# Kernel optimization log

Hardware: AMD Instinct MI355X
Metric: run time of the kernel (lower is better)

## Reference

```python
import jax, jax.numpy as jnp
import numpy as np

N = 100000      # nodes
E = 1600000     # edges (avg degree 16)
F_IN = 128      # dataset.num_features
H = 64          # hidden_channels
C = 40          # dataset.num_classes
LAYERS = 4      # number_conv_layers
EPS = 1e-12     # F.normalize eps


def _agnn_layer(x, src, dst):
    # AGNNConv with beta=1 (requires_grad=False):
    # alpha_ij = softmax_i( cos(x_i, x_j) ), out_i = sum_j alpha_ij * x_j
    xn = x / jnp.maximum(jnp.linalg.norm(x, axis=1, keepdims=True), EPS)
    logits = jnp.sum(xn[dst] * xn[src], axis=1)                      # [E]
    m = jax.lax.stop_gradient(jax.ops.segment_max(logits, dst, num_segments=N))
    e = jnp.exp(logits - m[dst])
    s = jax.ops.segment_sum(e, dst, num_segments=N)
    alpha = e / s[dst]                                               # [E]
    return jax.ops.segment_sum(alpha[:, None] * x[src], dst, num_segments=N)


def setup_inputs() -> dict:
    key = jax.random.key(0)
    k = jax.random.split(key, 6)
    x = jax.random.normal(k[0], (N, F_IN), dtype=jnp.float32)
    edge_index = jax.random.randint(k[1], (2, E), 0, N, dtype=jnp.int32)
    W1 = jax.random.normal(k[2], (F_IN, H), dtype=jnp.float32) * (1.0 / np.sqrt(F_IN))
    b1 = jnp.zeros((H,), dtype=jnp.float32)
    W2 = jax.random.normal(k[3], (H, C), dtype=jnp.float32) * (1.0 / np.sqrt(H))
    b2 = jnp.zeros((C,), dtype=jnp.float32)
    return {"x": x, "W1": W1, "b1": b1, "W2": W2, "b2": b2, "edge_index": edge_index}


def reference(x, W1, b1, W2, b2, edge_index):
    # add self loops (PyG AGNNConv default)
    loop = jnp.arange(N, dtype=edge_index.dtype)
    src = jnp.concatenate([edge_index[0], loop])
    dst = jnp.concatenate([edge_index[1], loop])
    h = jax.nn.relu(x @ W1 + b1)          # lin1 + relu (dropout p=0 / eval)
    for _ in range(LAYERS):
        h = _agnn_layer(h, src, dst)
    out = h @ W2 + b2                     # lin2
    return jax.nn.log_softmax(out, axis=1)
```

## Files before the change

kernel.cpp:

```cpp
#include <hip/hip_runtime.h>
#include <math.h>

#define F_IN 128
#define H_DIM 64
#define C_OUT 40
#define NBK 391
#define CHUNK 2048
#define XPAD 136
#define PHB 128
#define BCAP 5120

typedef _Float16 h8 __attribute__((ext_vector_type(8)));
typedef _Float16 half2t __attribute__((ext_vector_type(2)));
typedef float nf4 __attribute__((ext_vector_type(4)));
typedef _Float16 f16x8 __attribute__((ext_vector_type(8)));
typedef float f32x4 __attribute__((ext_vector_type(4)));

union H8 {
    h8 v;
    half2t p[4];
};

__device__ __forceinline__ float dot8(const H8& a, const H8& b) {
    float d = __builtin_amdgcn_fdot2(a.p[0], b.p[0], 0.0f, false);
    d = __builtin_amdgcn_fdot2(a.p[1], b.p[1], d, false);
    d = __builtin_amdgcn_fdot2(a.p[2], b.p[2], d, false);
    d = __builtin_amdgcn_fdot2(a.p[3], b.p[3], d, false);
    return d;
}

__device__ __forceinline__ float dpp_red8_add(float x) {
    int v = __builtin_bit_cast(int, x);
    x += __builtin_bit_cast(float, __builtin_amdgcn_update_dpp(0, v, 0xB1, 0xF, 0xF, true));
    v = __builtin_bit_cast(int, x);
    x += __builtin_bit_cast(float, __builtin_amdgcn_update_dpp(0, v, 0x4E, 0xF, 0xF, true));
    v = __builtin_bit_cast(int, x);
    x += __builtin_bit_cast(float, __builtin_amdgcn_update_dpp(0, v, 0x141, 0xF, 0xF, true));
    return x;
}


__global__ void __launch_bounds__(256) bphist_kernel(const int* __restrict__ dst,
                                                     int* __restrict__ part, int E,
                                                     const float* __restrict__ W1,
                                                     _Float16* __restrict__ w1t) {
    if (blockIdx.x >= PHB) {
        int t = (blockIdx.x - PHB) * 256 + threadIdx.x;
        if (t < F_IN * H_DIM) {
            int k = t >> 6, col = t & 63;
            w1t[col * F_IN + k] = (_Float16)W1[t];
        }
        return;
    }
    __shared__ int lh[512];
    int tid = threadIdx.x;
    lh[tid] = 0; lh[tid + 256] = 0;
    __syncthreads();
    int slice = (E + PHB - 1) / PHB;
    int lo = blockIdx.x * slice;
    int hi = min(E, lo + slice);
    for (int e = lo + tid; e < hi; e += 256) {
        int d = __builtin_nontemporal_load(&dst[e]);
        atomicAdd(&lh[d >> 8], 1);
    }
    __syncthreads();
    part[blockIdx.x * 512 + tid] = lh[tid];
    part[blockIdx.x * 512 + tid + 256] = lh[tid + 256];
}

__global__ void __launch_bounds__(512) bscan_kernel(const int* __restrict__ part,
                                                    int* __restrict__ bbase,
                                                    int* __restrict__ bcursor, int E) {
    __shared__ int sa[512], sb[512];
    int t = threadIdx.x;
    int v = 0;
#pragma unroll 4
    for (int b = 0; b < PHB; b++) v += part[b * 512 + t];
    sa[t] = v;
    __syncthreads();
    int* pa = sa; int* pb = sb;
#pragma unroll
    for (int off = 1; off < 512; off <<= 1) {
        pb[t] = pa[t] + ((t >= off) ? pa[t - off] : 0);
        __syncthreads();
        int* tmp = pa; pa = pb; pb = tmp;
    }
    if (t < NBK) {
        int excl = pa[t] - v;
        bbase[t] = excl;
        bcursor[t] = excl;
    }
    if (t == 0) bbase[NBK] = E;
}

__global__ void __launch_bounds__(512) binscatter_kernel(const int* __restrict__ src,
                                                         const int* __restrict__ dst,
                                                         int* __restrict__ bcursor,
                                                         unsigned int* __restrict__ pairs, int E) {
    __shared__ unsigned int sp[CHUNK];
    __shared__ unsigned short sbof[CHUNK];
    __shared__ int hist[512];
    __shared__ int scanA[512], scanB[512];
    __shared__ int cur[512];
    __shared__ int gbase[512];
    int tid = threadIdx.x;
    int e0 = blockIdx.x * CHUNK;
    int cnt = min(CHUNK, E - e0);

    int dv[CHUNK / 512], sv[CHUNK / 512];
#pragma unroll
    for (int i = 0; i < CHUNK / 512; i++) {
        int idx = tid + i * 512;
        if (idx < cnt) {
            dv[i] = __builtin_nontemporal_load(&dst[e0 + idx]);
            sv[i] = __builtin_nontemporal_load(&src[e0 + idx]);
        }
    }
    hist[tid] = 0;
    __syncthreads();
#pragma unroll
    for (int i = 0; i < CHUNK / 512; i++) {
        int idx = tid + i * 512;
        if (idx < cnt) atomicAdd(&hist[dv[i] >> 8], 1);
    }
    __syncthreads();
    scanA[tid] = hist[tid];
    __syncthreads();
    int* pa = scanA; int* pb = scanB;
#pragma unroll
    for (int off = 1; off < 512; off <<= 1) {
        pb[tid] = pa[tid] + ((tid >= off) ? pa[tid - off] : 0);
        __syncthreads();
        int* tmp = pa; pa = pb; pb = tmp;
    }
    cur[tid] = pa[tid] - hist[tid];
    __syncthreads();
#pragma unroll
    for (int i = 0; i < CHUNK / 512; i++) {
        int idx = tid + i * 512;
        if (idx < cnt) {
            int b = dv[i] >> 8;
            int lp = atomicAdd(&cur[b], 1);
            sp[lp] = ((unsigned int)(dv[i] & 255) << 24) | (unsigned int)sv[i];
            sbof[lp] = (unsigned short)b;
        }
    }
    {
        int c0 = hist[tid];
        gbase[tid] = c0 ? atomicAdd(&bcursor[tid], c0) : 0;
    }
    __syncthreads();
    for (int i = tid; i < cnt; i += 512) {
        int b = sbof[i];
        int off_in_b = i - (pa[b] - hist[b]);
        pairs[gbase[b] + off_in_b] = sp[i];
    }
}

__global__ void __launch_bounds__(512) bucketsort_kernel(const unsigned int* __restrict__ pairs,
                                                         const int* __restrict__ bbase,
                                                         int* __restrict__ rowptr,
                                                         int* __restrict__ ssrc, int N, int E) {
    __shared__ unsigned int spairs[BCAP];
    __shared__ int hist[256], scanA[256], scanB[256], cur[256];
    int b = blockIdx.x;
    int tid = threadIdx.x;
    int e0 = bbase[b], e1 = bbase[b + 1];
    int cnt = e1 - e0;
    bool lds = cnt <= BCAP;

    if (tid < 256) hist[tid] = 0;
    if (lds) {
        for (int i = tid; i < cnt; i += 512) spairs[i] = pairs[e0 + i];
    }
    __syncthreads();
    for (int i = tid; i < cnt; i += 512) {
        unsigned int p = lds ? spairs[i] : pairs[e0 + i];
        atomicAdd(&hist[p >> 24], 1);
    }
    __syncthreads();
    if (tid < 256) scanA[tid] = hist[tid];
    __syncthreads();
    int* pa = scanA; int* pb = scanB;
#pragma unroll
    for (int off = 1; off < 256; off <<= 1) {
        if (tid < 256) pb[tid] = pa[tid] + ((tid >= off) ? pa[tid - off] : 0);
        __syncthreads();
        int* tmp = pa; pa = pb; pb = tmp;
    }
    if (tid < 256) {
        int excl = pa[tid] - hist[tid];
        int node = (b << 8) + tid;
        if (node < N) rowptr[node] = e0 + excl;
        cur[tid] = e0 + excl;
    }
    if (b == NBK - 1 && tid == 0) rowptr[N] = E;
    __syncthreads();
    for (int i = tid; i < cnt; i += 512) {
        unsigned int p = lds ? spairs[i] : pairs[e0 + i];
        int pos = atomicAdd(&cur[p >> 24], 1);
        ssrc[pos] = (int)(p & 0x00FFFFFFu);
    }
}

__global__ void __launch_bounds__(256) lin1_kernel(
        const float* __restrict__ x, const _Float16* __restrict__ w1t,
        const float* __restrict__ b1, _Float16* __restrict__ hnout,
        float* __restrict__ nrmout, int n) {
    __shared__ _Float16 sx[64 * XPAD];
    __shared__ _Float16 sw[64 * XPAD];
    int tid = threadIdx.x;
    int r0 = blockIdx.x * 64;

    for (int ch = tid; ch < 64 * 32; ch += 256) {
        int row = ch >> 5, k4 = (ch & 31) << 2;
        float4 xv = make_float4(0.f, 0.f, 0.f, 0.f);
        if (r0 + row < n) xv = *(const float4*)(x + (size_t)(r0 + row) * F_IN + k4);
        _Float16* p = &sx[row * XPAD + k4];
        p[0] = (_Float16)xv.x; p[1] = (_Float16)xv.y;
        p[2] = (_Float16)xv.z; p[3] = (_Float16)xv.w;
    }
    for (int ch = tid; ch < 64 * 16; ch += 256) {
        int col = ch >> 4, k8 = (ch & 15) << 3;
        *(uint4*)&sw[col * XPAD + k8] = *(const uint4*)(w1t + col * F_IN + k8);
    }
    __syncthreads();

    int w = tid >> 6, lane = tid & 63;
    int q = lane >> 4, c = lane & 15;

    f16x8 afrag[4];
#pragma unroll
    for (int kk = 0; kk < 4; kk++)
        afrag[kk] = *(const f16x8*)&sx[(w * 16 + c) * XPAD + kk * 32 + q * 8];

    f32x4 acc[4] = {{0.f,0.f,0.f,0.f},{0.f,0.f,0.f,0.f},{0.f,0.f,0.f,0.f},{0.f,0.f,0.f,0.f}};
#pragma unroll
    for (int ct = 0; ct < 4; ct++) {
#pragma unroll
        for (int kk = 0; kk < 4; kk++) {
            f16x8 bfrag = *(const f16x8*)&sw[(ct * 16 + c) * XPAD + kk * 32 + q * 8];
            acc[ct] = __builtin_amdgcn_mfma_f32_16x16x32_f16(afrag[kk], bfrag, acc[ct], 0, 0, 0);
        }
    }

    float ss[4] = {0.f, 0.f, 0.f, 0.f};
#pragma unroll
    for (int ct = 0; ct < 4; ct++) {
        float bv = b1[ct * 16 + c];
#pragma unroll
        for (int r = 0; r < 4; r++) {
            float v = fmaxf(acc[ct][r] + bv, 0.0f);
            acc[ct][r] = v;
            ss[r] = fmaf(v, v, ss[r]);
        }
    }
#pragma unroll
    for (int k = 1; k < 16; k <<= 1) {
#pragma unroll
        for (int r = 0; r < 4; r++) ss[r] += __shfl_xor(ss[r], k, 64);
    }
    float nn[4], inv[4];
#pragma unroll
    for (int r = 0; r < 4; r++) {
        nn[r] = fmaxf(sqrtf(ss[r]), 1e-12f);
        inv[r] = 1.0f / nn[r];
    }
#pragma unroll
    for (int ct = 0; ct < 4; ct++)
#pragma unroll
        for (int r = 0; r < 4; r++)
            sx[(w * 16 + q * 4 + r) * XPAD + ct * 16 + c] = (_Float16)(acc[ct][r] * inv[r]);

    if (c == 0) {
#pragma unroll
        for (int r = 0; r < 4; r++) {
            int row = r0 + w * 16 + q * 4 + r;
            if (row < n) nrmout[row] = nn[r];
        }
    }
#pragma unroll
    for (int it = 0; it < 2; it++) {
        int row = w * 16 + it * 8 + (lane >> 3);
        int k8 = (lane & 7) * 8;
        if (r0 + row < n)
            *(uint4*)(hnout + (size_t)(r0 + row) * H_DIM + k8) =
                *(const uint4*)&sx[row * XPAD + k8];
    }
}

__global__ void __launch_bounds__(256, 3) agnn_kernel(
        const h8* __restrict__ h, const float* __restrict__ nrm,
        const int* __restrict__ rowptr, const int* __restrict__ ssrc,
        h8* __restrict__ hout, float* __restrict__ nrmout, int n, int E) {
    int wv = (blockIdx.x * blockDim.x + threadIdx.x) >> 6;
    int lane = threadIdx.x & 63;
    int g = lane >> 3;
    int sub = lane & 7;
    int wid = wv * 8 + g;
    bool nvalid = wid < n;
    int nid = nvalid ? wid : (n - 1);

    int e0 = rowptr[nid];
    int e1 = rowptr[nid + 1];
    int steps = nvalid ? (e1 - e0) : 0;
    int eclamp = min(max(e1 - 1, e0), E - 1);

    H8 hd; hd.v = h[(size_t)nid * 8 + sub];
    float ni = nrm[nid];

    int mx = steps;
    mx = max(mx, __shfl_xor(mx, 8, 64));
    mx = max(mx, __shfl_xor(mx, 16, 64));
    mx = max(mx, __shfl_xor(mx, 32, 64));

    float dself = dpp_red8_add(dot8(hd, hd));
    float wself = __expf(dself);
    float sw = wself;
    float aself = wself * ni;
    half2t ap = {(_Float16)aself, (_Float16)aself};
    half2t acc2[4];
#pragma unroll
    for (int j = 0; j < 4; j++) acc2[j] = ap * hd.p[j];

    int sA[8], sB[8];
    H8 XA[8], XB[8];
    float nA[8], nB[8];

    auto SLOAD = [&](int* s, int ofs) {
#pragma unroll
        for (int k = 0; k < 8; k++) s[k] = ssrc[min(e0 + ofs + k, eclamp)];
    };
    auto HLOAD = [&](const int* s, H8* X, float* xn) {
#pragma unroll
        for (int k = 0; k < 8; k++) {
            X[k].v = h[(size_t)s[k] * 8 + sub];
            xn[k] = nrm[s[k]];
        }
    };
    auto COMP = [&](const H8* X, const float* xn, int base) {
        float d[8];
#pragma unroll
        for (int k = 0; k < 8; k++) d[k] = dpp_red8_add(dot8(X[k], hd));
#pragma unroll
        for (int k = 0; k < 8; k++) {
            float wgt = (base + k < steps) ? __expf(d[k]) : 0.0f;
            sw += wgt;
            float a = wgt * xn[k];
            half2t apk = {(_Float16)a, (_Float16)a};
#pragma unroll
            for (int j = 0; j < 4; j++) acc2[j] += apk * X[k].p[j];
        }
    };

    int nb = (mx + 7) >> 3;
    SLOAD(sA, 0);
    __builtin_amdgcn_sched_barrier(0);
    HLOAD(sA, XA, nA);
    SLOAD(sB, 8);
    __builtin_amdgcn_sched_barrier(0);

    int base = 0;
    for (int b = 0; b < nb; b += 2) {
        HLOAD(sB, XB, nB);
        SLOAD(sA, base + 16);
        __builtin_amdgcn_sched_barrier(0);
        COMP(XA, nA, base);
        __builtin_amdgcn_sched_barrier(0);
        if (b + 1 >= nb) break;
        HLOAD(sA, XA, nA);
        SLOAD(sB, base + 24);
        __builtin_amdgcn_sched_barrier(0);
        COMP(XB, nB, base + 8);
        __builtin_amdgcn_sched_barrier(0);
        base += 16;
    }

    float inv = 1.0f / sw;
    float o[8];
#pragma unroll
    for (int j = 0; j < 4; j++) {
        o[2 * j] = (float)acc2[j][0] * inv;
        o[2 * j + 1] = (float)acc2[j][1] * inv;
    }
    float ss = 0.0f;
#pragma unroll
    for (int i = 0; i < 8; i++) ss = fmaf(o[i], o[i], ss);
    ss = dpp_red8_add(ss);
    float nn = fmaxf(sqrtf(ss), 1e-12f);
    float r = 1.0f / nn;
    h8 oh;
#pragma unroll
    for (int i = 0; i < 8; i++) oh[i] = (_Float16)(o[i] * r);
    if (nvalid) {
        hout[(size_t)wid * 8 + sub] = oh;
        if (sub == 0) nrmout[wid] = nn;
    }
}

__global__ void __launch_bounds__(256) lin2_kernel(
        const h8* __restrict__ h, const float* __restrict__ nrm,
        const float* __restrict__ W2, const float* __restrict__ b2,
        float* __restrict__ out, int n) {
    __shared__ h8 sh[32 * 8];
    __shared__ float snrm[32];
    int tid = threadIdx.x;
    int r0 = blockIdx.x * 32;
    int rows = min(32, n - r0);

    {
        const uint4* hg = (const uint4*)(h + (size_t)r0 * 8);
        uint4* sh4 = (uint4*)sh;
        int tot = rows * 8;
        for (int i = tid; i < tot; i += 256) sh4[i] = hg[i];
        if (tid < rows) snrm[tid] = nrm[r0 + tid];
    }
    __syncthreads();

    int wave = tid >> 6, lane = tid & 63;
    int rbase = wave * 8;

    float acc[8];
    if (lane < C_OUT) {
#pragma unroll
        for (int j = 0; j < 8; j++) acc[j] = 0.0f;
#pragma unroll 2
        for (int k = 0; k < H_DIM; k += 8) {
            float w[8];
#pragma unroll
            for (int i = 0; i < 8; i++) w[i] = W2[(k + i) * C_OUT + lane];
#pragma unroll
            for (int j = 0; j < 8; j++) {
                h8 hv = sh[(rbase + j) * 8 + (k >> 3)];
#pragma unroll
                for (int i = 0; i < 8; i++) acc[j] = fmaf((float)hv[i], w[i], acc[j]);
            }
        }
        float bl = b2[lane];
#pragma unroll
        for (int j = 0; j < 8; j++) acc[j] = fmaf(snrm[rbase + j], acc[j], bl);
    } else {
#pragma unroll
        for (int j = 0; j < 8; j++) acc[j] = -INFINITY;
    }

#pragma unroll
    for (int j = 0; j < 8; j++) {
        int r = rbase + j;
        if (r >= rows) break;
        float m = acc[j];
#pragma unroll
        for (int k = 1; k < 64; k <<= 1) m = fmaxf(m, __shfl_xor(m, k, 64));
        float e = (lane < C_OUT) ? __expf(acc[j] - m) : 0.0f;
        float s = e;
#pragma unroll
        for (int k = 1; k < 64; k <<= 1) s += __shfl_xor(s, k, 64);
        if (lane < C_OUT) out[(size_t)(r0 + r) * C_OUT + lane] = acc[j] - m - logf(s);
    }
}


extern "C" void kernel_launch(void* const* d_in, const int* in_sizes, int n_in,
                              void* d_out, int out_size, void* d_ws, size_t ws_size,
                              hipStream_t stream) {
    const float* x = (const float*)d_in[0];
    const float* W1 = (const float*)d_in[1];
    const float* b1 = (const float*)d_in[2];
    const float* W2 = (const float*)d_in[3];
    const float* b2 = (const float*)d_in[4];
    const int* ei = (const int*)d_in[5];

    const int N = in_sizes[0] / F_IN;
    const int E = in_sizes[5] / 2;
    const int* src = ei;
    const int* dst = ei + E;

    char* w = (char*)d_ws;
    auto carve = [&](size_t bytes) {
        char* p = w;
        w += (bytes + 255) & ~(size_t)255;
        return p;
    };
    _Float16* g1 = (_Float16*)carve((size_t)N * H_DIM * 2);
    _Float16* g2 = (_Float16*)carve((size_t)N * H_DIM * 2);
    float* rn1 = (float*)carve((size_t)N * 4);
    float* rn2 = (float*)carve((size_t)N * 4);
    int* rowptr = (int*)carve((size_t)(N + 1) * 4);
    int* bbase = (int*)carve(512 * 4);
    int* bcursor = (int*)carve(512 * 4);
    int* ssrc = (int*)carve((size_t)E * 4);
    _Float16* w1t = (_Float16*)carve((size_t)F_IN * H_DIM * 2);
    unsigned int* pairs = (unsigned int*)g2;
    int* part = (int*)g1;

    bphist_kernel<<<PHB + 32, 256, 0, stream>>>(dst, part, E, W1, w1t);
    bscan_kernel<<<1, 512, 0, stream>>>(part, bbase, bcursor, E);
    binscatter_kernel<<<(E + CHUNK - 1) / CHUNK, 512, 0, stream>>>(src, dst, bcursor, pairs, E);
    bucketsort_kernel<<<NBK, 512, 0, stream>>>(pairs, bbase, rowptr, ssrc, N, E);

    lin1_kernel<<<(N + 63) / 64, 256, 0, stream>>>(x, w1t, b1, g1, rn1, N);

    {
        int blocks = (N + 31) / 32;
        agnn_kernel<<<blocks, 256, 0, stream>>>((const h8*)g1, rn1, rowptr, ssrc, (h8*)g2, rn2, N, E);
        agnn_kernel<<<blocks, 256, 0, stream>>>((const h8*)g2, rn2, rowptr, ssrc, (h8*)g1, rn1, N, E);
        agnn_kernel<<<blocks, 256, 0, stream>>>((const h8*)g1, rn1, rowptr, ssrc, (h8*)g2, rn2, N, E);
        agnn_kernel<<<blocks, 256, 0, stream>>>((const h8*)g2, rn2, rowptr, ssrc, (h8*)g1, rn1, N, E);
    }

    lin2_kernel<<<(N + 31) / 32, 256, 0, stream>>>((const h8*)g1, rn1, W2, b2, (float*)d_out, N);
}
```

Baseline: 248.6 us.

## Drop per-node norm arrays and recompute norms from raw fp16 features per edge

Features are now stored unnormalized in fp16, and the separate per-node norm arrays are removed from lin1, all four AGNN layers and lin2. Each AGNN layer recomputes the destination norm once and each neighbour's norm on the fly from the gathered 8-lane row, using a dot product, a DPP reduction and rsqrt. The self-loop weight becomes the constant e, since a vector's cosine with itself is 1. This removes one scattered 4-byte gather per edge and the norm writes, at the cost of extra ALU and cross-lane reductions per edge. It also keeps unnormalized magnitudes in fp16, which carries some precision and range risk.

```diff
diff --git a/kernel.cpp b/kernel.cpp
--- a/kernel.cpp
+++ b/kernel.cpp
@@ -205,8 +205,7 @@
 
 __global__ void __launch_bounds__(256) lin1_kernel(
         const float* __restrict__ x, const _Float16* __restrict__ w1t,
-        const float* __restrict__ b1, _Float16* __restrict__ hnout,
-        float* __restrict__ nrmout, int n) {
+        const float* __restrict__ b1, _Float16* __restrict__ hnout, int n) {
     __shared__ _Float16 sx[64 * XPAD];
     __shared__ _Float16 sw[64 * XPAD];
     int tid = threadIdx.x;
@@ -244,41 +243,17 @@
         }
     }
 
-    float ss[4] = {0.f, 0.f, 0.f, 0.f};
+    __syncthreads();
 #pragma unroll
     for (int ct = 0; ct < 4; ct++) {
         float bv = b1[ct * 16 + c];
 #pragma unroll
         for (int r = 0; r < 4; r++) {
             float v = fmaxf(acc[ct][r] + bv, 0.0f);
-            acc[ct][r] = v;
-            ss[r] = fmaf(v, v, ss[r]);
-        }
-    }
-#pragma unroll
-    for (int k = 1; k < 16; k <<= 1) {
-#pragma unroll
-        for (int r = 0; r < 4; r++) ss[r] += __shfl_xor(ss[r], k, 64);
-    }
-    float nn[4], inv[4];
-#pragma unroll
-    for (int r = 0; r < 4; r++) {
-        nn[r] = fmaxf(sqrtf(ss[r]), 1e-12f);
-        inv[r] = 1.0f / nn[r];
-    }
-#pragma unroll
-    for (int ct = 0; ct < 4; ct++)
-#pragma unroll
-        for (int r = 0; r < 4; r++)
-            sx[(w * 16 + q * 4 + r) * XPAD + ct * 16 + c] = (_Float16)(acc[ct][r] * inv[r]);
-
-    if (c == 0) {
-#pragma unroll
-        for (int r = 0; r < 4; r++) {
-            int row = r0 + w * 16 + q * 4 + r;
-            if (row < n) nrmout[row] = nn[r];
-        }
-    }
+            sx[(w * 16 + q * 4 + r) * XPAD + ct * 16 + c] = (_Float16)v;
+        }
+    }
+    __syncthreads();
 #pragma unroll
     for (int it = 0; it < 2; it++) {
         int row = w * 16 + it * 8 + (lane >> 3);
@@ -290,9 +265,9 @@
 }
 
 __global__ void __launch_bounds__(256, 3) agnn_kernel(
-        const h8* __restrict__ h, const float* __restrict__ nrm,
+        const h8* __restrict__ h,
         const int* __restrict__ rowptr, const int* __restrict__ ssrc,
-        h8* __restrict__ hout, float* __restrict__ nrmout, int n, int E) {
+        h8* __restrict__ hout, int n, int E) {
     int wv = (blockIdx.x * blockDim.x + threadIdx.x) >> 6;
     int lane = threadIdx.x & 63;
     int g = lane >> 3;
@@ -307,47 +282,44 @@
     int eclamp = min(max(e1 - 1, e0), E - 1);
 
     H8 hd; hd.v = h[(size_t)nid * 8 + sub];
-    float ni = nrm[nid];
+    float nd2 = dpp_red8_add(dot8(hd, hd));
+    float rnd = rsqrtf(fmaxf(nd2, 1e-24f));
 
     int mx = steps;
     mx = max(mx, __shfl_xor(mx, 8, 64));
     mx = max(mx, __shfl_xor(mx, 16, 64));
     mx = max(mx, __shfl_xor(mx, 32, 64));
 
-    float dself = dpp_red8_add(dot8(hd, hd));
-    float wself = __expf(dself);
+    float wself = (nd2 > 0.0f) ? 2.71828182845904523f : 1.0f;
     float sw = wself;
-    float aself = wself * ni;
-    half2t ap = {(_Float16)aself, (_Float16)aself};
+    half2t ap = {(_Float16)wself, (_Float16)wself};
     half2t acc2[4];
 #pragma unroll
     for (int j = 0; j < 4; j++) acc2[j] = ap * hd.p[j];
 
     int sA[8], sB[8];
     H8 XA[8], XB[8];
-    float nA[8], nB[8];
 
     auto SLOAD = [&](int* s, int ofs) {
 #pragma unroll
         for (int k = 0; k < 8; k++) s[k] = ssrc[min(e0 + ofs + k, eclamp)];
     };
-    auto HLOAD = [&](const int* s, H8* X, float* xn) {
+    auto HLOAD = [&](const int* s, H8* X) {
+#pragma unroll
+        for (int k = 0; k < 8; k++) X[k].v = h[(size_t)s[k] * 8 + sub];
+    };
+    auto COMP = [&](const H8* X, int base) {
+        float s2[8], d[8];
+#pragma unroll
+        for (int k = 0; k < 8; k++) s2[k] = dpp_red8_add(dot8(X[k], X[k]));
+#pragma unroll
+        for (int k = 0; k < 8; k++) d[k] = dpp_red8_add(dot8(X[k], hd));
 #pragma unroll
         for (int k = 0; k < 8; k++) {
-            X[k].v = h[(size_t)s[k] * 8 + sub];
-            xn[k] = nrm[s[k]];
-        }
-    };
-    auto COMP = [&](const H8* X, const float* xn, int base) {
-        float d[8];
-#pragma unroll
-        for (int k = 0; k < 8; k++) d[k] = dpp_red8_add(dot8(X[k], hd));
-#pragma unroll
-        for (int k = 0; k < 8; k++) {
-            float wgt = (base + k < steps) ? __expf(d[k]) : 0.0f;
+            float rs = rsqrtf(fmaxf(s2[k], 1e-24f));
+            float wgt = (base + k < steps) ? __expf(d[k] * rnd * rs) : 0.0f;
             sw += wgt;
-            float a = wgt * xn[k];
-            half2t apk = {(_Float16)a, (_Float16)a};
+            half2t apk = {(_Float16)wgt, (_Float16)wgt};
 #pragma unroll
             for (int j = 0; j < 4; j++) acc2[j] += apk * X[k].p[j];
         }
@@ -356,54 +328,41 @@
     int nb = (mx + 7) >> 3;
     SLOAD(sA, 0);
     __builtin_amdgcn_sched_barrier(0);
-    HLOAD(sA, XA, nA);
+    HLOAD(sA, XA);
     SLOAD(sB, 8);
     __builtin_amdgcn_sched_barrier(0);
 
     int base = 0;
     for (int b = 0; b < nb; b += 2) {
-        HLOAD(sB, XB, nB);
+        HLOAD(sB, XB);
         SLOAD(sA, base + 16);
         __builtin_amdgcn_sched_barrier(0);
-        COMP(XA, nA, base);
+        COMP(XA, base);
         __builtin_amdgcn_sched_barrier(0);
         if (b + 1 >= nb) break;
-        HLOAD(sA, XA, nA);
+        HLOAD(sA, XA);
         SLOAD(sB, base + 24);
         __builtin_amdgcn_sched_barrier(0);
-        COMP(XB, nB, base + 8);
+        COMP(XB, base + 8);
         __builtin_amdgcn_sched_barrier(0);
         base += 16;
     }
 
     float inv = 1.0f / sw;
-    float o[8];
+    h8 oh;
 #pragma unroll
     for (int j = 0; j < 4; j++) {
-        o[2 * j] = (float)acc2[j][0] * inv;
-        o[2 * j + 1] = (float)acc2[j][1] * inv;
-    }
-    float ss = 0.0f;
-#pragma unroll
-    for (int i = 0; i < 8; i++) ss = fmaf(o[i], o[i], ss);
-    ss = dpp_red8_add(ss);
-    float nn = fmaxf(sqrtf(ss), 1e-12f);
-    float r = 1.0f / nn;
-    h8 oh;
-#pragma unroll
-    for (int i = 0; i < 8; i++) oh[i] = (_Float16)(o[i] * r);
-    if (nvalid) {
-        hout[(size_t)wid * 8 + sub] = oh;
-        if (sub == 0) nrmout[wid] = nn;
-    }
+        oh[2 * j] = (_Float16)((float)acc2[j][0] * inv);
+        oh[2 * j + 1] = (_Float16)((float)acc2[j][1] * inv);
+    }
+    if (nvalid) hout[(size_t)wid * 8 + sub] = oh;
 }
 
 __global__ void __launch_bounds__(256) lin2_kernel(
-        const h8* __restrict__ h, const float* __restrict__ nrm,
+        const h8* __restrict__ h,
         const float* __restrict__ W2, const float* __restrict__ b2,
         float* __restrict__ out, int n) {
     __shared__ h8 sh[32 * 8];
-    __shared__ float snrm[32];
     int tid = threadIdx.x;
     int r0 = blockIdx.x * 32;
     int rows = min(32, n - r0);
@@ -413,7 +372,6 @@
         uint4* sh4 = (uint4*)sh;
         int tot = rows * 8;
         for (int i = tid; i < tot; i += 256) sh4[i] = hg[i];
-        if (tid < rows) snrm[tid] = nrm[r0 + tid];
     }
     __syncthreads();
 
@@ -438,7 +396,7 @@
         }
         float bl = b2[lane];
 #pragma unroll
-        for (int j = 0; j < 8; j++) acc[j] = fmaf(snrm[rbase + j], acc[j], bl);
+        for (int j = 0; j < 8; j++) acc[j] += bl;
     } else {
 #pragma unroll
         for (int j = 0; j < 8; j++) acc[j] = -INFINITY;
@@ -483,8 +441,6 @@
     };
     _Float16* g1 = (_Float16*)carve((size_t)N * H_DIM * 2);
     _Float16* g2 = (_Float16*)carve((size_t)N * H_DIM * 2);
-    float* rn1 = (float*)carve((size_t)N * 4);
-    float* rn2 = (float*)carve((size_t)N * 4);
     int* rowptr = (int*)carve((size_t)(N + 1) * 4);
     int* bbase = (int*)carve(512 * 4);
     int* bcursor = (int*)carve(512 * 4);
@@ -498,15 +454,15 @@
     binscatter_kernel<<<(E + CHUNK - 1) / CHUNK, 512, 0, stream>>>(src, dst, bcursor, pairs, E);
     bucketsort_kernel<<<NBK, 512, 0, stream>>>(pairs, bbase, rowptr, ssrc, N, E);
 
-    lin1_kernel<<<(N + 63) / 64, 256, 0, stream>>>(x, w1t, b1, g1, rn1, N);
+    lin1_kernel<<<(N + 63) / 64, 256, 0, stream>>>(x, w1t, b1, g1, N);
 
     {
         int blocks = (N + 31) / 32;
-        agnn_kernel<<<blocks, 256, 0, stream>>>((const h8*)g1, rn1, rowptr, ssrc, (h8*)g2, rn2, N, E);
-        agnn_kernel<<<blocks, 256, 0, stream>>>((const h8*)g2, rn2, rowptr, ssrc, (h8*)g1, rn1, N, E);
-        agnn_kernel<<<blocks, 256, 0, stream>>>((const h8*)g1, rn1, rowptr, ssrc, (h8*)g2, rn2, N, E);
-        agnn_kernel<<<blocks, 256, 0, stream>>>((const h8*)g2, rn2, rowptr, ssrc, (h8*)g1, rn1, N, E);
-    }
-
-    lin2_kernel<<<(N + 31) / 32, 256, 0, stream>>>((const h8*)g1, rn1, W2, b2, (float*)d_out, N);
-}
+        agnn_kernel<<<blocks, 256, 0, stream>>>((const h8*)g1, rowptr, ssrc, (h8*)g2, N, E);
+        agnn_kernel<<<blocks, 256, 0, stream>>>((const h8*)g2, rowptr, ssrc, (h8*)g1, N, E);
+        agnn_kernel<<<blocks, 256, 0, stream>>>((const h8*)g1, rowptr, ssrc, (h8*)g2, N, E);
+        agnn_kernel<<<blocks, 256, 0, stream>>>((const h8*)g2, rowptr, ssrc, (h8*)g1, N, E);
+    }
+
+    lin2_kernel<<<(N + 31) / 32, 256, 0, stream>>>((const h8*)g1, W2, b2, (float*)d_out, N);
+}
```

New measurement: 252.1 us. Within noise of the previous version (+1.4%).
